# Kernel optimization log

Measured on AMD Instinct MI355X. Metric: run time of the kernel, lower is better.

## Reference

```python
import jax, jax.numpy as jnp
import numpy as np

NUM_RNA = 1927
N_NODES = 100000
N_EDGES = 1600000
IN_C, HID_C, OUT_C = 128, 128, 64
EPS = 1e-5  # BatchNorm1d default eps


def gcn_conv(x, W, b, src, dst, num_nodes):
    """PyG GCNConv: linear transform, add self-loops, symmetric-normalized scatter-add."""
    h = x @ W  # [N, C_out]
    loop = jnp.arange(num_nodes, dtype=src.dtype)
    s = jnp.concatenate([src, loop])  # self-loops appended
    d = jnp.concatenate([dst, loop])
    deg = jax.ops.segment_sum(jnp.ones(d.shape[0], dtype=h.dtype), d, num_segments=num_nodes)
    dinv = jnp.where(deg > 0, jax.lax.rsqrt(deg), jnp.zeros_like(deg))
    norm = dinv[s] * dinv[d]  # [E+N]
    msg = h[s] * norm[:, None]  # [E+N, C_out] gather (memory-bound)
    out = jax.ops.segment_sum(msg, d, num_segments=num_nodes)  # scatter-add
    return out + b


def batchnorm(x, gamma, beta):
    # training-mode BatchNorm1d: batch stats over node dim, biased variance
    mu = jnp.mean(x, axis=0)
    var = jnp.mean(jnp.square(x - mu), axis=0)
    return (x - mu) * jax.lax.rsqrt(var + EPS) * gamma + beta


def setup_inputs() -> dict:
    key = jax.random.key(0)
    ks = jax.random.split(key, 6)
    x = jax.random.normal(ks[0], (N_NODES, IN_C), dtype=jnp.float32)
    edge_index = jax.random.randint(ks[1], (2, N_EDGES), 0, N_NODES)
    # xavier_uniform for conv weights
    lim1 = float(np.sqrt(6.0 / (IN_C + HID_C)))
    lim2 = float(np.sqrt(6.0 / (HID_C + OUT_C)))
    W1 = jax.random.uniform(ks[2], (IN_C, HID_C), minval=-lim1, maxval=lim1, dtype=jnp.float32)
    W2 = jax.random.uniform(ks[3], (HID_C, OUT_C), minval=-lim2, maxval=lim2, dtype=jnp.float32)
    b1 = jnp.zeros((HID_C,), dtype=jnp.float32)
    b2 = jnp.zeros((OUT_C,), dtype=jnp.float32)
    gamma1 = jnp.ones((HID_C,), dtype=jnp.float32)
    beta1 = jnp.zeros((HID_C,), dtype=jnp.float32)
    gamma2 = jnp.ones((OUT_C,), dtype=jnp.float32)
    beta2 = jnp.zeros((OUT_C,), dtype=jnp.float32)
    return {"x": x, "edge_index": edge_index, "W1": W1, "b1": b1,
            "gamma1": gamma1, "beta1": beta1, "W2": W2, "b2": b2,
            "gamma2": gamma2, "beta2": beta2}


def reference(x, edge_index, W1, b1, gamma1, beta1, W2, b2, gamma2, beta2):
    src, dst = edge_index[0], edge_index[1]
    h = gcn_conv(x, W1, b1, src, dst, N_NODES)
    h = jax.nn.relu(batchnorm(h, gamma1, beta1))
    h = gcn_conv(h, W2, b2, src, dst, N_NODES)
    h = batchnorm(h, gamma2, beta2)
    return h[:NUM_RNA], h[NUM_RNA:]
```

## Files before the change

### kernel.cpp

```cpp
#include <hip/hip_runtime.h>
#include <hip/hip_bf16.h>


#define IN_C 128
#define HID_C 128
#define OUT_C2 64
#define BN_EPS 1e-5f

typedef __attribute__((ext_vector_type(8))) short short8v;
typedef __attribute__((ext_vector_type(4))) float float4v;
typedef __attribute__((ext_vector_type(4))) int int4v;

__device__ inline ushort f2bf(float f) {
    union { float f; unsigned u; } x; x.f = f;
    return (ushort)((x.u + 0x7fffu + ((x.u >> 16) & 1u)) >> 16);
}
__device__ inline float bf2f(ushort u) {
    union { unsigned u; float f; } x; x.u = ((unsigned)u) << 16;
    return x.f;
}

__global__ void init_kernel(float* __restrict__ ws) {
    int i = blockIdx.x * blockDim.x + threadIdx.x;
    if (i < 1296) ws[i] = 0.0f;
}

template <int OC>
__device__ inline void wreorder_impl(const float* __restrict__ W,
                                     ushort* __restrict__ wfrag, int t) {
    constexpr int NCT = OC / 16;
    int lane = t & 63;
    int rest = t >> 6;
    int ct = rest % NCT;
    int kk = rest / NCT;
    int col = ct * 16 + (lane & 15);
    int krow = kk * 32 + (lane >> 4) * 8;
    ushort tmp[8];
    #pragma unroll
    for (int e = 0; e < 8; ++e)
        tmp[e] = f2bf(W[(size_t)(krow + e) * OC + col]);
    uint4 st;
    st.x = (uint)tmp[0] | ((uint)tmp[1] << 16);
    st.y = (uint)tmp[2] | ((uint)tmp[3] << 16);
    st.z = (uint)tmp[4] | ((uint)tmp[5] << 16);
    st.w = (uint)tmp[6] | ((uint)tmp[7] << 16);
    *(uint4*)&wfrag[(size_t)t * 8] = st;
}

__global__ __launch_bounds__(256) void bucket_count_kernel(
    const int* __restrict__ dst, int* __restrict__ bcnt, int E, int nbA,
    const float* __restrict__ W1, const float* __restrict__ W2,
    ushort* __restrict__ wf1, ushort* __restrict__ wf2)
{
    if (blockIdx.x >= nbA) {
        int b = blockIdx.x - nbA;
        if (b < 8) wreorder_impl<HID_C>(W1, wf1, b * 256 + threadIdx.x);
        else       wreorder_impl<OUT_C2>(W2, wf2, (b - 8) * 256 + threadIdx.x);
        return;
    }
    __shared__ int h[512];
    int t = threadIdx.x;
    h[t] = 0; h[t + 256] = 0;
    __syncthreads();
    int i0 = blockIdx.x * 1024 + t * 4;
    if (i0 < E) {
        int4v d = __builtin_nontemporal_load((const int4v*)&dst[i0]);
        atomicAdd(&h[d.x >> 8], 1);
        atomicAdd(&h[d.y >> 8], 1);
        atomicAdd(&h[d.z >> 8], 1);
        atomicAdd(&h[d.w >> 8], 1);
    }
    __syncthreads();
    if (h[t])       atomicAdd(&bcnt[t], h[t]);
    if (h[t + 256]) atomicAdd(&bcnt[t + 256], h[t + 256]);
}

__global__ __launch_bounds__(256) void bucket_scan_kernel(
    int* __restrict__ bcnt, int* __restrict__ bbase,
    int* __restrict__ row_ptr, int E, int N)
{
    __shared__ int sd[512];
    int t = threadIdx.x;
    int a = bcnt[t], b = bcnt[t + 256];
    sd[t] = a; sd[t + 256] = b;
    __syncthreads();
    for (int off = 1; off < 512; off <<= 1) {
        int v0 = (t >= off) ? sd[t - off] : 0;
        int v1 = sd[t + 256 - off];
        __syncthreads();
        sd[t] += v0; sd[t + 256] += v1;
        __syncthreads();
    }
    int e0 = sd[t] - a, e1 = sd[t + 256] - b;
    bbase[t] = e0; bbase[t + 256] = e1;
    bcnt[t] = e0; bcnt[t + 256] = e1;
    if (t == 0) row_ptr[N] = E;
}

__global__ __launch_bounds__(256) void bucket_scatter_kernel(
    const int* __restrict__ src, const int* __restrict__ dst,
    int* __restrict__ bcursor, int2* __restrict__ pairs, int E)
{
    __shared__ int h[512];
    __shared__ int gb[512];
    int t = threadIdx.x;
    h[t] = 0; h[t + 256] = 0;
    __syncthreads();
    int i0 = blockIdx.x * 1024 + t * 4;
    bool act = i0 < E;
    int4v d, s;
    int bk0 = 0, bk1 = 0, bk2 = 0, bk3 = 0, r0 = 0, r1 = 0, r2 = 0, r3 = 0;
    if (act) {
        d = __builtin_nontemporal_load((const int4v*)&dst[i0]);
        s = __builtin_nontemporal_load((const int4v*)&src[i0]);
        bk0 = d.x >> 8; r0 = atomicAdd(&h[bk0], 1);
        bk1 = d.y >> 8; r1 = atomicAdd(&h[bk1], 1);
        bk2 = d.z >> 8; r2 = atomicAdd(&h[bk2], 1);
        bk3 = d.w >> 8; r3 = atomicAdd(&h[bk3], 1);
    }
    __syncthreads();
    if (h[t])       gb[t] = atomicAdd(&bcursor[t], h[t]);
    if (h[t + 256]) gb[t + 256] = atomicAdd(&bcursor[t + 256], h[t + 256]);
    __syncthreads();
    if (act) {
        pairs[gb[bk0] + r0] = make_int2(s.x, d.x);
        pairs[gb[bk1] + r1] = make_int2(s.y, d.y);
        pairs[gb[bk2] + r2] = make_int2(s.z, d.z);
        pairs[gb[bk3] + r3] = make_int2(s.w, d.w);
    }
}

__global__ __launch_bounds__(256) void bucket_csr_kernel(
    const int2* __restrict__ pairs, const int* __restrict__ bbase,
    int* __restrict__ csr_src, int* __restrict__ row_ptr,
    float* __restrict__ dinv, int N)
{
    __shared__ int cnt[256];
    __shared__ int sd[256];
    int t = threadIdx.x;
    int node0 = blockIdx.x << 8;
    int base = bbase[blockIdx.x], end = bbase[blockIdx.x + 1];
    cnt[t] = 0;
    __syncthreads();
    for (int i = base + t; i < end; i += 256)
        atomicAdd(&cnt[pairs[i].y & 255], 1);
    __syncthreads();
    int myc = cnt[t];
    sd[t] = myc;
    __syncthreads();
    for (int off = 1; off < 256; off <<= 1) {
        int v = (t >= off) ? sd[t - off] : 0;
        __syncthreads();
        sd[t] += v;
        __syncthreads();
    }
    int ofs = sd[t] - myc;
    int node = node0 + t;
    if (node < N) {
        row_ptr[node] = base + ofs;
        dinv[node] = rsqrtf((float)myc + 1.0f);
    }
    cnt[t] = ofs;
    __syncthreads();
    for (int i = base + t; i < end; i += 256) {
        int2 p = pairs[i];
        int pos = atomicAdd(&cnt[p.y & 255], 1);
        csr_src[base + pos] = p.x;
    }
}

template <int OC, bool BN_IN>
__global__ __launch_bounds__(256) void mfma_gemm_kernel(
    const void* __restrict__ Xv, const ushort* __restrict__ wfrag,
    ushort* __restrict__ Y, const float* __restrict__ dinv,
    const float* __restrict__ sc, const float* __restrict__ sh, int N)
{
    constexpr int NCT = OC / 16;
    int wave = (blockIdx.x * 256 + threadIdx.x) >> 6;
    int lane = threadIdx.x & 63;
    int row16 = wave * 16;
    if (row16 >= N) return;
    int r = lane & 15;
    int g = lane >> 4;
    int row = row16 + r;

    float4v acc[NCT];
    #pragma unroll
    for (int ct = 0; ct < NCT; ++ct) acc[ct] = (float4v){0.f, 0.f, 0.f, 0.f};

    const short8v* wf = (const short8v*)wfrag;

    #pragma unroll
    for (int kk = 0; kk < 4; ++kk) {
        int k0 = kk * 32 + g * 8;
        short8v a;
        if constexpr (!BN_IN) {
            const float* xp = (const float*)Xv + (size_t)row * 128 + k0;
            float4 x0 = *(const float4*)xp;
            float4 x1 = *(const float4*)(xp + 4);
            a[0] = (short)f2bf(x0.x); a[1] = (short)f2bf(x0.y);
            a[2] = (short)f2bf(x0.z); a[3] = (short)f2bf(x0.w);
            a[4] = (short)f2bf(x1.x); a[5] = (short)f2bf(x1.y);
            a[6] = (short)f2bf(x1.z); a[7] = (short)f2bf(x1.w);
        } else {
            const ushort* xp = (const ushort*)Xv + (size_t)row * 128 + k0;
            uint4 v = *(const uint4*)xp;
            float4 s0 = *(const float4*)&sc[k0];
            float4 s1 = *(const float4*)&sc[k0 + 4];
            float4 h0 = *(const float4*)&sh[k0];
            float4 h1 = *(const float4*)&sh[k0 + 4];
            a[0] = (short)f2bf(fmaxf(fmaf(bf2f((ushort)(v.x & 0xffff)), s0.x, h0.x), 0.f));
            a[1] = (short)f2bf(fmaxf(fmaf(bf2f((ushort)(v.x >> 16)),    s0.y, h0.y), 0.f));
            a[2] = (short)f2bf(fmaxf(fmaf(bf2f((ushort)(v.y & 0xffff)), s0.z, h0.z), 0.f));
            a[3] = (short)f2bf(fmaxf(fmaf(bf2f((ushort)(v.y >> 16)),    s0.w, h0.w), 0.f));
            a[4] = (short)f2bf(fmaxf(fmaf(bf2f((ushort)(v.z & 0xffff)), s1.x, h1.x), 0.f));
            a[5] = (short)f2bf(fmaxf(fmaf(bf2f((ushort)(v.z >> 16)),    s1.y, h1.y), 0.f));
            a[6] = (short)f2bf(fmaxf(fmaf(bf2f((ushort)(v.w & 0xffff)), s1.z, h1.z), 0.f));
            a[7] = (short)f2bf(fmaxf(fmaf(bf2f((ushort)(v.w >> 16)),    s1.w, h1.w), 0.f));
        }
        #pragma unroll
        for (int ct = 0; ct < NCT; ++ct) {
            short8v b = wf[((size_t)(kk * NCT + ct)) * 64 + lane];
            acc[ct] = __builtin_amdgcn_mfma_f32_16x16x32_bf16(a, b, acc[ct], 0, 0, 0);
        }
    }
    float di[4];
    #pragma unroll
    for (int i = 0; i < 4; ++i) di[i] = dinv[row16 + g * 4 + i];
    #pragma unroll
    for (int ct = 0; ct < NCT; ++ct) {
        #pragma unroll
        for (int i = 0; i < 4; ++i) {
            int orow = row16 + g * 4 + i;
            Y[(size_t)orow * OC + ct * 16 + r] = f2bf(acc[ct][i] * di[i]);
        }
    }
}

template <int C>
__global__ __launch_bounds__(256) void aggregate_kernel(
    const ushort* __restrict__ h, const int* __restrict__ row_ptr,
    const int* __restrict__ csr_src, const float* __restrict__ dinv,
    ushort* __restrict__ out, int N)
{
    constexpr int TPN = C / 8;
    constexpr int PAR = 64 / TPN;
    int wid = (blockIdx.x * 256 + threadIdx.x) >> 6;
    if (wid >= N) return;
    int lane = threadIdx.x & 63;
    int part = lane / TPN;
    int c0 = (lane % TPN) * 8;
    float acc[8] = {0.f, 0.f, 0.f, 0.f, 0.f, 0.f, 0.f, 0.f};

    uint4 vself = make_uint4(0u, 0u, 0u, 0u);
    if (part == 0) vself = *(const uint4*)&h[(size_t)wid * C + c0];

    int e = row_ptr[wid] + part;
    int e1 = row_ptr[wid + 1];
    for (; e + PAR < e1; e += 2 * PAR) {
        int s0 = __builtin_nontemporal_load(&csr_src[e]);
        int s1 = __builtin_nontemporal_load(&csr_src[e + PAR]);
        uint4 v0 = *(const uint4*)&h[(size_t)s0 * C + c0];
        uint4 v1 = *(const uint4*)&h[(size_t)s1 * C + c0];
        acc[0] += bf2f((ushort)(v0.x & 0xffff)) + bf2f((ushort)(v1.x & 0xffff));
        acc[1] += bf2f((ushort)(v0.x >> 16))    + bf2f((ushort)(v1.x >> 16));
        acc[2] += bf2f((ushort)(v0.y & 0xffff)) + bf2f((ushort)(v1.y & 0xffff));
        acc[3] += bf2f((ushort)(v0.y >> 16))    + bf2f((ushort)(v1.y >> 16));
        acc[4] += bf2f((ushort)(v0.z & 0xffff)) + bf2f((ushort)(v1.z & 0xffff));
        acc[5] += bf2f((ushort)(v0.z >> 16))    + bf2f((ushort)(v1.z >> 16));
        acc[6] += bf2f((ushort)(v0.w & 0xffff)) + bf2f((ushort)(v1.w & 0xffff));
        acc[7] += bf2f((ushort)(v0.w >> 16))    + bf2f((ushort)(v1.w >> 16));
    }
    if (e < e1) {
        int s = __builtin_nontemporal_load(&csr_src[e]);
        uint4 v = *(const uint4*)&h[(size_t)s * C + c0];
        acc[0] += bf2f((ushort)(v.x & 0xffff));
        acc[1] += bf2f((ushort)(v.x >> 16));
        acc[2] += bf2f((ushort)(v.y & 0xffff));
        acc[3] += bf2f((ushort)(v.y >> 16));
        acc[4] += bf2f((ushort)(v.z & 0xffff));
        acc[5] += bf2f((ushort)(v.z >> 16));
        acc[6] += bf2f((ushort)(v.w & 0xffff));
        acc[7] += bf2f((ushort)(v.w >> 16));
    }
    if (part == 0) {
        acc[0] += bf2f((ushort)(vself.x & 0xffff));
        acc[1] += bf2f((ushort)(vself.x >> 16));
        acc[2] += bf2f((ushort)(vself.y & 0xffff));
        acc[3] += bf2f((ushort)(vself.y >> 16));
        acc[4] += bf2f((ushort)(vself.z & 0xffff));
        acc[5] += bf2f((ushort)(vself.z >> 16));
        acc[6] += bf2f((ushort)(vself.w & 0xffff));
        acc[7] += bf2f((ushort)(vself.w >> 16));
    }
    #pragma unroll
    for (int off = TPN; off < 64; off <<= 1) {
        #pragma unroll
        for (int j = 0; j < 8; ++j)
            acc[j] += __shfl_xor(acc[j], off, 64);
    }
    if (part == 0) {
        float dd = dinv[wid];
        uint4 st;
        #pragma unroll
        for (int j = 0; j < 8; ++j) acc[j] *= dd;
        st.x = (uint)f2bf(acc[0]) | ((uint)f2bf(acc[1]) << 16);
        st.y = (uint)f2bf(acc[2]) | ((uint)f2bf(acc[3]) << 16);
        st.z = (uint)f2bf(acc[4]) | ((uint)f2bf(acc[5]) << 16);
        st.w = (uint)f2bf(acc[6]) | ((uint)f2bf(acc[7]) << 16);
        *(uint4*)&out[(size_t)wid * C + c0] = st;
    }
}

template <int C>
__global__ __launch_bounds__(256) void stats_prep_kernel(
    const ushort* __restrict__ h, float* __restrict__ sums ,
    const float* __restrict__ gamma, const float* __restrict__ beta,
    float* __restrict__ sc, float* __restrict__ sh,
    int* __restrict__ ticket, int nblocks, int N)
{
    constexpr int CG = C / 8;
    constexpr int RPB = 256 / CG;
    __shared__ float red[RPB][CG][16];
    __shared__ bool lastblk;
    int tid = threadIdx.x;
    int cg = tid % CG, rg = tid / CG;
    int c0 = cg * 8;
    float s[8] = {0.f,0.f,0.f,0.f,0.f,0.f,0.f,0.f};
    float q[8] = {0.f,0.f,0.f,0.f,0.f,0.f,0.f,0.f};
    for (int r = blockIdx.x * RPB + rg; r < N; r += gridDim.x * RPB) {
        uint4 v = *(const uint4*)&h[(size_t)r * C + c0];
        float f0 = bf2f((ushort)(v.x & 0xffff)), f1 = bf2f((ushort)(v.x >> 16));
        float f2 = bf2f((ushort)(v.y & 0xffff)), f3 = bf2f((ushort)(v.y >> 16));
        float f4 = bf2f((ushort)(v.z & 0xffff)), f5 = bf2f((ushort)(v.z >> 16));
        float f6 = bf2f((ushort)(v.w & 0xffff)), f7 = bf2f((ushort)(v.w >> 16));
        s[0]+=f0; s[1]+=f1; s[2]+=f2; s[3]+=f3; s[4]+=f4; s[5]+=f5; s[6]+=f6; s[7]+=f7;
        q[0]=fmaf(f0,f0,q[0]); q[1]=fmaf(f1,f1,q[1]); q[2]=fmaf(f2,f2,q[2]); q[3]=fmaf(f3,f3,q[3]);
        q[4]=fmaf(f4,f4,q[4]); q[5]=fmaf(f5,f5,q[5]); q[6]=fmaf(f6,f6,q[6]); q[7]=fmaf(f7,f7,q[7]);
    }
    #pragma unroll
    for (int j = 0; j < 8; ++j) { red[rg][cg][j] = s[j]; red[rg][cg][8 + j] = q[j]; }
    __syncthreads();
    if (rg == 0) {
        float a[16];
        #pragma unroll
        for (int i = 0; i < 16; ++i) a[i] = red[0][cg][i];
        for (int r2 = 1; r2 < RPB; ++r2)
            #pragma unroll
            for (int i = 0; i < 16; ++i) a[i] += red[r2][cg][i];
        #pragma unroll
        for (int j = 0; j < 8; ++j) {
            atomicAdd(&sums[c0 + j], a[j]);
            atomicAdd(&sums[C + c0 + j], a[8 + j]);
        }
    }
    __syncthreads();
    if (tid == 0) {
        __threadfence();
        int old = atomicAdd(ticket, 1);
        lastblk = (old == nblocks - 1);
    }
    __syncthreads();
    if (lastblk && tid < C) {
        float sv = atomicAdd(&sums[tid], 0.0f);
        float qv = atomicAdd(&sums[C + tid], 0.0f);
        float invN = 1.0f / (float)N;
        float mu = sv * invN;
        float var = qv * invN - mu * mu;
        float scl = rsqrtf(var + BN_EPS) * gamma[tid];
        sc[tid] = scl;
        sh[tid] = beta[tid] - mu * scl;
    }
}

__global__ void bn_apply_kernel(const ushort* __restrict__ in, float* __restrict__ out,
                                const float* __restrict__ sc, const float* __restrict__ sh,
                                int N)
{
    int total = N * (OUT_C2 / 8);
    int i = blockIdx.x * blockDim.x + threadIdx.x;
    int stride = gridDim.x * blockDim.x;
    for (; i < total; i += stride) {
        int c0 = (i & 7) * 8;
        uint4 v = *(const uint4*)&in[(size_t)i * 8];
        float4 s0 = *(const float4*)&sc[c0];
        float4 s1 = *(const float4*)&sc[c0 + 4];
        float4 h0 = *(const float4*)&sh[c0];
        float4 h1 = *(const float4*)&sh[c0 + 4];
        float4 o0, o1;
        o0.x = fmaf(bf2f((ushort)(v.x & 0xffff)), s0.x, h0.x);
        o0.y = fmaf(bf2f((ushort)(v.x >> 16)),    s0.y, h0.y);
        o0.z = fmaf(bf2f((ushort)(v.y & 0xffff)), s0.z, h0.z);
        o0.w = fmaf(bf2f((ushort)(v.y >> 16)),    s0.w, h0.w);
        o1.x = fmaf(bf2f((ushort)(v.z & 0xffff)), s1.x, h1.x);
        o1.y = fmaf(bf2f((ushort)(v.z >> 16)),    s1.y, h1.y);
        o1.z = fmaf(bf2f((ushort)(v.w & 0xffff)), s1.z, h1.z);
        o1.w = fmaf(bf2f((ushort)(v.w >> 16)),    s1.w, h1.w);
        *(float4*)&out[(size_t)i * 8] = o0;
        *(float4*)&out[(size_t)i * 8 + 4] = o1;
    }
}

extern "C" void kernel_launch(void* const* d_in, const int* in_sizes, int n_in,
                              void* d_out, int out_size, void* d_ws, size_t ws_size,
                              hipStream_t stream) {
    const float* x      = (const float*)d_in[0];
    const int*   ei     = (const int*)d_in[1];
    const float* W1     = (const float*)d_in[2];
    const float* gamma1 = (const float*)d_in[4];
    const float* beta1  = (const float*)d_in[5];
    const float* W2     = (const float*)d_in[6];
    const float* gamma2 = (const float*)d_in[8];
    const float* beta2  = (const float*)d_in[9];

    const int N = in_sizes[0] / IN_C;
    const int E = in_sizes[1] / 2;
    const int* src = ei;
    const int* dst = ei + E;
    const int nbA   = (E + 1023) / 1024;
    const int nbuck = (N + 255) >> 8;

    float* ws      = (float*)d_ws;
    float* stats1  = ws;
    float* stats2  = ws + 256;
    float* sc1     = ws + 384;
    float* sh1     = ws + 512;
    float* sc2     = ws + 640;
    float* sh2     = ws + 704;
    int*   ticket1 = (int*)(ws + 768);
    int*   ticket2 = (int*)(ws + 769);
    int*   bcnt    = (int*)(ws + 784);
    int*   bbase   = (int*)(ws + 1296);
    float* dinv    = ws + 1824;
    int*   row_ptr = (int*)(dinv + N);
    int*   csr_src = row_ptr + N + 16;
    ushort* wfrag1 = (ushort*)(csr_src + E);
    ushort* wfrag2 = wfrag1 + 16384;
    ushort* h1     = wfrag2 + 8192;
    ushort* bufB   = h1 + (size_t)N * HID_C;
    ushort* h2     = bufB + (size_t)N * HID_C;
    ushort* agg2b  = h2 + (size_t)N * OUT_C2;
    int2*  pairs   = (int2*)h2;

    const int nbGemm = (N / 16 + 3) / 4;

    init_kernel<<<6, 256, 0, stream>>>(ws);
    bucket_count_kernel<<<nbA + 12, 256, 0, stream>>>(dst, bcnt, E, nbA,
                                                      W1, W2, wfrag1, wfrag2);
    bucket_scan_kernel<<<1, 256, 0, stream>>>(bcnt, bbase, row_ptr, E, N);
    bucket_scatter_kernel<<<nbA, 256, 0, stream>>>(src, dst, bcnt, pairs, E);
    bucket_csr_kernel<<<nbuck, 256, 0, stream>>>(pairs, bbase, csr_src, row_ptr,
                                                 dinv, N);

    mfma_gemm_kernel<HID_C, false><<<nbGemm, 256, 0, stream>>>(
        x, wfrag1, h1, dinv, nullptr, nullptr, N);
    aggregate_kernel<HID_C><<<(N + 3) / 4, 256, 0, stream>>>(
        h1, row_ptr, csr_src, dinv, bufB, N);
    stats_prep_kernel<HID_C><<<256, 256, 0, stream>>>(
        bufB, stats1, gamma1, beta1, sc1, sh1, ticket1, 256, N);

    mfma_gemm_kernel<OUT_C2, true><<<nbGemm, 256, 0, stream>>>(
        bufB, wfrag2, h2, dinv, sc1, sh1, N);
    aggregate_kernel<OUT_C2><<<(N + 3) / 4, 256, 0, stream>>>(
        h2, row_ptr, csr_src, dinv, agg2b, N);
    stats_prep_kernel<OUT_C2><<<256, 256, 0, stream>>>(
        agg2b, stats2, gamma2, beta2, sc2, sh2, ticket2, 256, N);

    bn_apply_kernel<<<2048, 256, 0, stream>>>(agg2b, (float*)d_out, sc2, sh2, N);
}
```

Before: 406.3 us.

## Fold bucket scan into scatter/CSR kernels and fuse final BN stats with apply

Drops the single-block bucket scan launch. Every scatter and CSR block now recomputes the 512-entry prefix sum locally and uses a separate zeroed cursor array. The final BN statistics and apply kernels are merged into one 256-block kernel that uses a ticket plus a spin-wait flag as a grid barrier, and the first GEMM's x loads become nontemporal. This saves two launches and their gaps, in exchange for redundant per-block scans and a spin barrier that needs all 256 blocks resident at once.

Result: faster. 396.5 us (-2.4%).

```diff
diff --git a/kernel.cpp b/kernel.cpp
--- a/kernel.cpp
+++ b/kernel.cpp
@@ -22,7 +22,7 @@
 
 __global__ void init_kernel(float* __restrict__ ws) {
     int i = blockIdx.x * blockDim.x + threadIdx.x;
-    if (i < 1296) ws[i] = 0.0f;
+    if (i < 1808) ws[i] = 0.0f;
 }
 
 template <int OC>
@@ -75,35 +75,28 @@
     if (h[t + 256]) atomicAdd(&bcnt[t + 256], h[t + 256]);
 }
 
-__global__ __launch_bounds__(256) void bucket_scan_kernel(
-    int* __restrict__ bcnt, int* __restrict__ bbase,
-    int* __restrict__ row_ptr, int E, int N)
-{
-    __shared__ int sd[512];
-    int t = threadIdx.x;
-    int a = bcnt[t], b = bcnt[t + 256];
-    sd[t] = a; sd[t + 256] = b;
-    __syncthreads();
-    for (int off = 1; off < 512; off <<= 1) {
-        int v0 = (t >= off) ? sd[t - off] : 0;
-        int v1 = sd[t + 256 - off];
-        __syncthreads();
-        sd[t] += v0; sd[t + 256] += v1;
-        __syncthreads();
-    }
-    int e0 = sd[t] - a, e1 = sd[t + 256] - b;
-    bbase[t] = e0; bbase[t + 256] = e1;
-    bcnt[t] = e0; bcnt[t + 256] = e1;
-    if (t == 0) row_ptr[N] = E;
-}
-
 __global__ __launch_bounds__(256) void bucket_scatter_kernel(
     const int* __restrict__ src, const int* __restrict__ dst,
-    int* __restrict__ bcursor, int2* __restrict__ pairs, int E)
-{
+    const int* __restrict__ bcnt, int* __restrict__ bcursor,
+    int2* __restrict__ pairs, int E)
+{
+    __shared__ int bs[512];
     __shared__ int h[512];
     __shared__ int gb[512];
     int t = threadIdx.x;
+    int a = bcnt[t], b = bcnt[t + 256];
+    bs[t] = a; bs[t + 256] = b;
+    __syncthreads();
+    for (int off = 1; off < 512; off <<= 1) {
+        int v0 = (t >= off) ? bs[t - off] : 0;
+        int v1 = bs[t + 256 - off];
+        __syncthreads();
+        bs[t] += v0; bs[t + 256] += v1;
+        __syncthreads();
+    }
+    int e0 = bs[t] - a, e1 = bs[t + 256] - b;
+    __syncthreads();
+    bs[t] = e0; bs[t + 256] = e1;
     h[t] = 0; h[t + 256] = 0;
     __syncthreads();
     int i0 = blockIdx.x * 1024 + t * 4;
@@ -119,8 +112,8 @@
         bk3 = d.w >> 8; r3 = atomicAdd(&h[bk3], 1);
     }
     __syncthreads();
-    if (h[t])       gb[t] = atomicAdd(&bcursor[t], h[t]);
-    if (h[t + 256]) gb[t + 256] = atomicAdd(&bcursor[t + 256], h[t + 256]);
+    if (h[t])       gb[t] = bs[t] + atomicAdd(&bcursor[t], h[t]);
+    if (h[t + 256]) gb[t + 256] = bs[t + 256] + atomicAdd(&bcursor[t + 256], h[t + 256]);
     __syncthreads();
     if (act) {
         pairs[gb[bk0] + r0] = make_int2(s.x, d.x);
@@ -131,15 +124,32 @@
 }
 
 __global__ __launch_bounds__(256) void bucket_csr_kernel(
-    const int2* __restrict__ pairs, const int* __restrict__ bbase,
+    const int2* __restrict__ pairs, const int* __restrict__ bcnt,
     int* __restrict__ csr_src, int* __restrict__ row_ptr,
-    float* __restrict__ dinv, int N)
-{
+    float* __restrict__ dinv, int E, int N)
+{
+    __shared__ int bs[512];
     __shared__ int cnt[256];
     __shared__ int sd[256];
     int t = threadIdx.x;
+    int a = bcnt[t], b = bcnt[t + 256];
+    bs[t] = a; bs[t + 256] = b;
+    __syncthreads();
+    for (int off = 1; off < 512; off <<= 1) {
+        int v0 = (t >= off) ? bs[t - off] : 0;
+        int v1 = bs[t + 256 - off];
+        __syncthreads();
+        bs[t] += v0; bs[t + 256] += v1;
+        __syncthreads();
+    }
+    int e0 = bs[t] - a, e1 = bs[t + 256] - b;
+    __syncthreads();
+    bs[t] = e0; bs[t + 256] = e1;
+    __syncthreads();
     int node0 = blockIdx.x << 8;
-    int base = bbase[blockIdx.x], end = bbase[blockIdx.x + 1];
+    int base = bs[blockIdx.x];
+    int end  = (blockIdx.x == 511) ? E : bs[blockIdx.x + 1];
+    if (blockIdx.x == 0 && t == 0) row_ptr[N] = E;
     cnt[t] = 0;
     __syncthreads();
     for (int i = base + t; i < end; i += 256)
@@ -196,12 +206,12 @@
         short8v a;
         if constexpr (!BN_IN) {
             const float* xp = (const float*)Xv + (size_t)row * 128 + k0;
-            float4 x0 = *(const float4*)xp;
-            float4 x1 = *(const float4*)(xp + 4);
-            a[0] = (short)f2bf(x0.x); a[1] = (short)f2bf(x0.y);
-            a[2] = (short)f2bf(x0.z); a[3] = (short)f2bf(x0.w);
-            a[4] = (short)f2bf(x1.x); a[5] = (short)f2bf(x1.y);
-            a[6] = (short)f2bf(x1.z); a[7] = (short)f2bf(x1.w);
+            float4v x0 = __builtin_nontemporal_load((const float4v*)xp);
+            float4v x1 = __builtin_nontemporal_load((const float4v*)(xp + 4));
+            a[0] = (short)f2bf(x0[0]); a[1] = (short)f2bf(x0[1]);
+            a[2] = (short)f2bf(x0[2]); a[3] = (short)f2bf(x0[3]);
+            a[4] = (short)f2bf(x1[0]); a[5] = (short)f2bf(x1[1]);
+            a[6] = (short)f2bf(x1[2]); a[7] = (short)f2bf(x1[3]);
         } else {
             const ushort* xp = (const ushort*)Xv + (size_t)row * 128 + k0;
             uint4 v = *(const uint4*)xp;
@@ -373,29 +383,91 @@
     }
 }
 
-__global__ void bn_apply_kernel(const ushort* __restrict__ in, float* __restrict__ out,
-                                const float* __restrict__ sc, const float* __restrict__ sh,
-                                int N)
-{
-    int total = N * (OUT_C2 / 8);
-    int i = blockIdx.x * blockDim.x + threadIdx.x;
-    int stride = gridDim.x * blockDim.x;
-    for (; i < total; i += stride) {
-        int c0 = (i & 7) * 8;
-        uint4 v = *(const uint4*)&in[(size_t)i * 8];
-        float4 s0 = *(const float4*)&sc[c0];
-        float4 s1 = *(const float4*)&sc[c0 + 4];
-        float4 h0 = *(const float4*)&sh[c0];
-        float4 h1 = *(const float4*)&sh[c0 + 4];
+__global__ __launch_bounds__(256) void stats2_bn_kernel(
+    const ushort* __restrict__ h, float* __restrict__ sums ,
+    const float* __restrict__ gamma, const float* __restrict__ beta,
+    float* __restrict__ sc, float* __restrict__ sh,
+    int* __restrict__ ticket, int* __restrict__ flag,
+    float* __restrict__ out, int nblocks, int N)
+{
+    constexpr int C = OUT_C2;
+    constexpr int CG = C / 8;
+    constexpr int RPB = 256 / CG;
+    __shared__ float red[RPB][CG][16];
+    __shared__ bool lastblk;
+    __shared__ float lsc[C], lsh[C];
+    int tid = threadIdx.x;
+    int cg = tid % CG, rg = tid / CG;
+    int c0 = cg * 8;
+    float s[8] = {0.f,0.f,0.f,0.f,0.f,0.f,0.f,0.f};
+    float q[8] = {0.f,0.f,0.f,0.f,0.f,0.f,0.f,0.f};
+    for (int r = blockIdx.x * RPB + rg; r < N; r += gridDim.x * RPB) {
+        uint4 v = *(const uint4*)&h[(size_t)r * C + c0];
+        float f0 = bf2f((ushort)(v.x & 0xffff)), f1 = bf2f((ushort)(v.x >> 16));
+        float f2 = bf2f((ushort)(v.y & 0xffff)), f3 = bf2f((ushort)(v.y >> 16));
+        float f4 = bf2f((ushort)(v.z & 0xffff)), f5 = bf2f((ushort)(v.z >> 16));
+        float f6 = bf2f((ushort)(v.w & 0xffff)), f7 = bf2f((ushort)(v.w >> 16));
+        s[0]+=f0; s[1]+=f1; s[2]+=f2; s[3]+=f3; s[4]+=f4; s[5]+=f5; s[6]+=f6; s[7]+=f7;
+        q[0]=fmaf(f0,f0,q[0]); q[1]=fmaf(f1,f1,q[1]); q[2]=fmaf(f2,f2,q[2]); q[3]=fmaf(f3,f3,q[3]);
+        q[4]=fmaf(f4,f4,q[4]); q[5]=fmaf(f5,f5,q[5]); q[6]=fmaf(f6,f6,q[6]); q[7]=fmaf(f7,f7,q[7]);
+    }
+    #pragma unroll
+    for (int j = 0; j < 8; ++j) { red[rg][cg][j] = s[j]; red[rg][cg][8 + j] = q[j]; }
+    __syncthreads();
+    if (rg == 0) {
+        float a[16];
+        #pragma unroll
+        for (int i = 0; i < 16; ++i) a[i] = red[0][cg][i];
+        for (int r2 = 1; r2 < RPB; ++r2)
+            #pragma unroll
+            for (int i = 0; i < 16; ++i) a[i] += red[r2][cg][i];
+        #pragma unroll
+        for (int j = 0; j < 8; ++j) {
+            atomicAdd(&sums[c0 + j], a[j]);
+            atomicAdd(&sums[C + c0 + j], a[8 + j]);
+        }
+    }
+    __syncthreads();
+    if (tid == 0) {
+        __threadfence();
+        int old = atomicAdd(ticket, 1);
+        lastblk = (old == nblocks - 1);
+    }
+    __syncthreads();
+    if (lastblk) {
+        if (tid < C) {
+            float sv = atomicAdd(&sums[tid], 0.0f);
+            float qv = atomicAdd(&sums[C + tid], 0.0f);
+            float invN = 1.0f / (float)N;
+            float mu = sv * invN;
+            float var = qv * invN - mu * mu;
+            float scl = rsqrtf(var + BN_EPS) * gamma[tid];
+            atomicAdd(&sc[tid], scl);
+            atomicAdd(&sh[tid], beta[tid] - mu * scl);
+        }
+        __syncthreads();
+        if (tid == 0) { __threadfence(); atomicAdd(flag, 1); }
+    }
+    if (tid == 0) {
+        while (atomicAdd(flag, 0) == 0) __builtin_amdgcn_s_sleep(2);
+    }
+    __syncthreads();
+    if (tid < C)          lsc[tid] = atomicAdd(&sc[tid], 0.0f);
+    else if (tid < 2 * C) lsh[tid - C] = atomicAdd(&sh[tid - C], 0.0f);
+    __syncthreads();
+    int total = N * (C / 8);
+    for (int i = blockIdx.x * 256 + tid; i < total; i += gridDim.x * 256) {
+        int cc = (i & 7) * 8;
+        uint4 v = *(const uint4*)&h[(size_t)i * 8];
         float4 o0, o1;
-        o0.x = fmaf(bf2f((ushort)(v.x & 0xffff)), s0.x, h0.x);
-        o0.y = fmaf(bf2f((ushort)(v.x >> 16)),    s0.y, h0.y);
-        o0.z = fmaf(bf2f((ushort)(v.y & 0xffff)), s0.z, h0.z);
-        o0.w = fmaf(bf2f((ushort)(v.y >> 16)),    s0.w, h0.w);
-        o1.x = fmaf(bf2f((ushort)(v.z & 0xffff)), s1.x, h1.x);
-        o1.y = fmaf(bf2f((ushort)(v.z >> 16)),    s1.y, h1.y);
-        o1.z = fmaf(bf2f((ushort)(v.w & 0xffff)), s1.z, h1.z);
-        o1.w = fmaf(bf2f((ushort)(v.w >> 16)),    s1.w, h1.w);
+        o0.x = fmaf(bf2f((ushort)(v.x & 0xffff)), lsc[cc + 0], lsh[cc + 0]);
+        o0.y = fmaf(bf2f((ushort)(v.x >> 16)),    lsc[cc + 1], lsh[cc + 1]);
+        o0.z = fmaf(bf2f((ushort)(v.y & 0xffff)), lsc[cc + 2], lsh[cc + 2]);
+        o0.w = fmaf(bf2f((ushort)(v.y >> 16)),    lsc[cc + 3], lsh[cc + 3]);
+        o1.x = fmaf(bf2f((ushort)(v.z & 0xffff)), lsc[cc + 4], lsh[cc + 4]);
+        o1.y = fmaf(bf2f((ushort)(v.z >> 16)),    lsc[cc + 5], lsh[cc + 5]);
+        o1.z = fmaf(bf2f((ushort)(v.w & 0xffff)), lsc[cc + 6], lsh[cc + 6]);
+        o1.w = fmaf(bf2f((ushort)(v.w >> 16)),    lsc[cc + 7], lsh[cc + 7]);
         *(float4*)&out[(size_t)i * 8] = o0;
         *(float4*)&out[(size_t)i * 8 + 4] = o1;
     }
@@ -429,9 +501,10 @@
     float* sh2     = ws + 704;
     int*   ticket1 = (int*)(ws + 768);
     int*   ticket2 = (int*)(ws + 769);
+    int*   flag2   = (int*)(ws + 770);
     int*   bcnt    = (int*)(ws + 784);
-    int*   bbase   = (int*)(ws + 1296);
-    float* dinv    = ws + 1824;
+    int*   bcursor = (int*)(ws + 1296);
+    float* dinv    = ws + 1808;
     int*   row_ptr = (int*)(dinv + N);
     int*   csr_src = row_ptr + N + 16;
     ushort* wfrag1 = (ushort*)(csr_src + E);
@@ -444,13 +517,12 @@
 
     const int nbGemm = (N / 16 + 3) / 4;
 
-    init_kernel<<<6, 256, 0, stream>>>(ws);
+    init_kernel<<<8, 256, 0, stream>>>(ws);
     bucket_count_kernel<<<nbA + 12, 256, 0, stream>>>(dst, bcnt, E, nbA,
                                                       W1, W2, wfrag1, wfrag2);
-    bucket_scan_kernel<<<1, 256, 0, stream>>>(bcnt, bbase, row_ptr, E, N);
-    bucket_scatter_kernel<<<nbA, 256, 0, stream>>>(src, dst, bcnt, pairs, E);
-    bucket_csr_kernel<<<nbuck, 256, 0, stream>>>(pairs, bbase, csr_src, row_ptr,
-                                                 dinv, N);
+    bucket_scatter_kernel<<<nbA, 256, 0, stream>>>(src, dst, bcnt, bcursor, pairs, E);
+    bucket_csr_kernel<<<nbuck, 256, 0, stream>>>(pairs, bcnt, csr_src, row_ptr,
+                                                 dinv, E, N);
 
     mfma_gemm_kernel<HID_C, false><<<nbGemm, 256, 0, stream>>>(
         x, wfrag1, h1, dinv, nullptr, nullptr, N);
@@ -463,8 +535,7 @@
         bufB, wfrag2, h2, dinv, sc1, sh1, N);
     aggregate_kernel<OUT_C2><<<(N + 3) / 4, 256, 0, stream>>>(
         h2, row_ptr, csr_src, dinv, agg2b, N);
-    stats_prep_kernel<OUT_C2><<<256, 256, 0, stream>>>(
-        agg2b, stats2, gamma2, beta2, sc2, sh2, ticket2, 256, N);
-
-    bn_apply_kernel<<<2048, 256, 0, stream>>>(agg2b, (float*)d_out, sc2, sh2, N);
-}
+    stats2_bn_kernel<<<256, 256, 0, stream>>>(
+        agg2b, stats2, gamma2, beta2, sc2, sh2, ticket2, flag2,
+        (float*)d_out, 256, N);
+}
```
